# Performance work log

Hardware: AMD Instinct MI355X
Metric: run time of the kernel (lower is better)

## Reference

```python
import jax, jax.numpy as jnp
import numpy as np

BIG = 1e9
GRAPH_LAYERS = 2
FLOW_ITERS = 10
DUAL_ITERS = 10
STEP = 0.1
MOM = 0.9


def _forward(node_features, node_embeddings, demands, adj, neighborhoods,
             enc_W0, enc_b0, enc_W1, enc_b1,
             attn_W, attn_a_src, attn_a_dst, nbr_q,
             gru_W, gru_U, gru_b,
             dec_W0, dec_b0, dec_W1, dec_b1,
             dual_W0, dual_b0, dual_W1, dual_b1):
    E = enc_W1.shape[1]
    K = neighborhoods.shape[0]
    # --- node encoder MLP (tanh, activate_final=True) ---
    x = jnp.concatenate([node_embeddings, node_features], axis=-1)  # [B,N,Fin]
    h = jnp.tanh(jnp.tanh(x @ enc_W0 + enc_b0) @ enc_W1 + enc_b1)   # [B,N,E]
    attn_coefs = None
    for _ in range(GRAPH_LAYERS):
        # --- AttentionNeighborhood: multi-head GAT per hop level, then attention over levels ---
        z = jnp.einsum('bnd,hde->hbne', h, attn_W)                   # [H,B,N,E]
        s_src = jnp.einsum('hbne,he->hbn', z, attn_a_src)
        s_dst = jnp.einsum('hbne,he->hbn', z, attn_a_dst)
        scores = jnp.tanh(s_src[:, :, :, None] + s_dst[:, :, None, :])  # [H,B,N,N]
        aggs = []
        for k in range(K):
            masked = jnp.where(neighborhoods[k][None] > 0, scores, -BIG)
            alpha = jax.nn.softmax(masked, axis=-1)                  # [H,B,N,N]
            agg = jnp.tanh(jnp.einsum('hbnm,hbme->hbne', alpha, z).mean(axis=0))  # heads averaged -> [B,N,E]
            aggs.append(agg)
        aggs = jnp.stack(aggs, axis=2)                               # [B,N,K,E]
        attn_coefs = jax.nn.softmax(jnp.tanh(jnp.einsum('bnke,e->bnk', aggs, nbr_q)), axis=-1)
        nxt = jnp.einsum('bnk,bnke->bne', attn_coefs, aggs)          # [B,N,E]
        # --- GRU state update (tanh activation) ---
        zr = jax.nn.sigmoid(nxt @ gru_W[:, :2 * E] + h @ gru_U[:, :2 * E] + gru_b[:2 * E])
        zg, r = zr[..., :E], zr[..., E:]
        h_tilde = jnp.tanh(nxt @ gru_W[:, 2 * E:] + (r * h) @ gru_U[:, 2 * E:] + gru_b[2 * E:])
        h = (1.0 - zg) * h + zg * h_tilde
    # --- flow-proportion decoder + masked softmax over neighbors ---
    node_weights = jnp.tanh(h @ dec_W0 + dec_b0) @ dec_W1 + dec_b1   # [B,N,1]
    pred = adj * jnp.swapaxes(node_weights, 1, 2)                    # adj * node_weights^T
    weights = -BIG * (1.0 - adj) + pred
    prop = jax.nn.softmax(weights, axis=-1)                          # [B,N,N]
    # --- iterative min-cost-flow solver ---
    def mcf_step(flow, _):
        inflow = flow.sum(axis=1)[:, :, None]                        # inflow_i = sum_j flow[j,i]
        return prop * jax.nn.relu(inflow - demands), None
    flow, _ = jax.lax.scan(mcf_step, jnp.zeros_like(prop), None, length=FLOW_ITERS)
    # should_correct_flows: cancel opposing flow on each edge pair
    flow = flow - adj * jnp.minimum(flow, jnp.swapaxes(flow, 1, 2))
    flow_cost = jnp.sum(flow * flow, axis=(1, 2))                    # square cost, per graph
    # --- dual decoder + projected momentum ascent dual-flow solver ---
    dual_vars = jnp.tanh(h @ dual_W0 + dual_b0) @ dual_W1 + dual_b1  # [B,N,1]
    dual_diff = adj * (dual_vars - jnp.swapaxes(dual_vars, 1, 2))    # [B,N,N]
    def dual_step(carry, _):
        y, m = carry
        g = 2.0 * y - dual_diff                                      # d/dy [y^2 - dual_diff*y]
        m = MOM * m + g
        y = adj * jax.nn.relu(y - STEP * m)
        return (y, m), None
    (dflow, _m), _ = jax.lax.scan(dual_step,
                                  (jnp.zeros_like(dual_diff), jnp.zeros_like(dual_diff)),
                                  None, length=DUAL_ITERS)
    dual_demand = jnp.sum(dual_vars * demands, axis=(1, 2))
    dual_cost = jnp.sum(dflow * dflow - dual_diff * dflow, axis=(1, 2)) - dual_demand
    return flow_cost - dual_cost                                     # primal-dual gap loss, [B]


def setup_inputs() -> dict:
    key = jax.random.key(0)
    ks = jax.random.split(key, 24)
    B, N, Femb, Ffeat, E, H = 2, 2048, 16, 2, 64, 2
    Fin = Femb + Ffeat
    node_embeddings = jax.random.normal(ks[0], (B, N, Femb), jnp.float32)
    node_features = jax.random.normal(ks[1], (B, N, Ffeat), jnp.float32)
    d = jax.random.normal(ks[2], (B, N, 1), jnp.float32) * 0.1
    demands = d - d.mean(axis=1, keepdims=True)                      # balanced demands
    eye = jnp.eye(N, dtype=jnp.float32)
    u = jax.random.uniform(ks[3], (B, N, N))
    adj = (u < 0.008).astype(jnp.float32) * (1.0 - eye)              # avg degree ~16
    a2 = (jnp.matmul(adj, adj) > 0).astype(jnp.float32) * (1.0 - eye)
    neighborhoods = jnp.stack([adj, a2], axis=0)                     # [K,B,N,N]
    def init(k, fan_in, shape):
        return jax.random.normal(k, shape, jnp.float32) / jnp.sqrt(float(fan_in))
    return {
        'node_features': node_features, 'node_embeddings': node_embeddings,
        'demands': demands, 'adj': adj, 'neighborhoods': neighborhoods,
        'enc_W0': init(ks[4], Fin, (Fin, 64)), 'enc_b0': jnp.zeros((64,)),
        'enc_W1': init(ks[5], 64, (64, E)), 'enc_b1': jnp.zeros((E,)),
        'attn_W': init(ks[6], E, (H, E, E)),
        'attn_a_src': init(ks[7], E, (H, E)), 'attn_a_dst': init(ks[8], E, (H, E)),
        'nbr_q': init(ks[9], E, (E,)),
        'gru_W': init(ks[10], E, (E, 3 * E)), 'gru_U': init(ks[11], E, (E, 3 * E)),
        'gru_b': jnp.zeros((3 * E,)),
        'dec_W0': init(ks[12], E, (E, 64)), 'dec_b0': jnp.zeros((64,)),
        'dec_W1': init(ks[13], 64, (64, 1)), 'dec_b1': jnp.zeros((1,)),
        'dual_W0': init(ks[14], E, (E, 64)), 'dual_b0': jnp.zeros((64,)),
        'dual_W1': init(ks[15], 64, (64, 1)), 'dual_b1': jnp.zeros((1,)),
    }


def reference(node_features, node_embeddings, demands, adj, neighborhoods,
              enc_W0, enc_b0, enc_W1, enc_b1,
              attn_W, attn_a_src, attn_a_dst, nbr_q,
              gru_W, gru_U, gru_b,
              dec_W0, dec_b0, dec_W1, dec_b1,
              dual_W0, dual_b0, dual_W1, dual_b1):
    return _forward(node_features, node_embeddings, demands, adj, neighborhoods,
                    enc_W0, enc_b0, enc_W1, enc_b1,
                    attn_W, attn_a_src, attn_a_dst, nbr_q,
                    gru_W, gru_U, gru_b,
                    dec_W0, dec_b0, dec_W1, dec_b1,
                    dual_W0, dual_b0, dual_W1, dual_b1)
```

## Files before the change

kernel.cpp:

```cpp
#include <hip/hip_runtime.h>

#define B_ 2
#define N_ 2048
#define E_ 64
#define FIN_ 18
#define ADJ_CAP 128
#define A2_CAP 1024
#define DR 16

__device__ __forceinline__ float wave_sum(float v) {
  #pragma unroll
  for (int o = 32; o > 0; o >>= 1) v += __shfl_xor(v, o);
  return v;
}
__device__ __forceinline__ float wave_max(float v) {
  #pragma unroll
  for (int o = 32; o > 0; o >>= 1) v = fmaxf(v, __shfl_xor(v, o));
  return v;
}
__device__ __forceinline__ void grp_reduce(float4& a) {
  #pragma unroll
  for (int o = 16; o <= 32; o <<= 1) {
    a.x += __shfl_xor(a.x, o); a.y += __shfl_xor(a.y, o);
    a.z += __shfl_xor(a.z, o); a.w += __shfl_xor(a.w, o);
  }
}

__global__ void k_csr_adj(const float* __restrict__ nbhd, int* __restrict__ adj_idx,
                          int* __restrict__ adj_cnt, unsigned* __restrict__ amask,
                          float* __restrict__ accum, int* __restrict__ tcnt) {
  int wv = threadIdx.x >> 6;
  int row = blockIdx.x * 4 + wv;
  int lane = threadIdx.x & 63;
  if (row == 0 && lane < 8) accum[lane] = 0.f;
  if (lane == 0) tcnt[row] = 0;
  __shared__ unsigned M[4][64];
  M[wv][lane] = 0;
  const float* r = nbhd + (size_t)row * N_;
  int* idx = adj_idx + (size_t)row * ADJ_CAP;
  int cnt = 0;
  unsigned long long below = (1ull << lane) - 1ull;
  for (int j0 = 0; j0 < N_; j0 += 256) {
    float4 v = ((const float4*)(r + j0))[lane];
    bool p0 = v.x > 0.f, p1 = v.y > 0.f, p2 = v.z > 0.f, p3 = v.w > 0.f;
    unsigned long long b0 = __ballot(p0), b1 = __ballot(p1),
                       b2 = __ballot(p2), b3 = __ballot(p3);
    int pos = cnt + __popcll(b0 & below) + __popcll(b1 & below) +
              __popcll(b2 & below) + __popcll(b3 & below);
    int base_j = j0 + lane * 4;
    if (p0) { if (pos < ADJ_CAP) idx[pos] = base_j;     pos++; }
    if (p1) { if (pos < ADJ_CAP) idx[pos] = base_j + 1; pos++; }
    if (p2) { if (pos < ADJ_CAP) idx[pos] = base_j + 2; pos++; }
    if (p3) { if (pos < ADJ_CAP) idx[pos] = base_j + 3; pos++; }
    unsigned nib = (p0 ? 1u : 0u) | (p1 ? 2u : 0u) | (p2 ? 4u : 0u) | (p3 ? 8u : 0u);
    if (nib) atomicOr(&M[wv][(j0 >> 5) + (lane >> 3)], nib << ((lane & 7) * 4));
    cnt += __popcll(b0) + __popcll(b1) + __popcll(b2) + __popcll(b3);
  }
  if (lane == 0) adj_cnt[row] = (cnt < ADJ_CAP) ? cnt : ADJ_CAP;
  amask[(size_t)row * 64 + lane] = M[wv][lane];
}

__global__ __launch_bounds__(64) void k_a2(
    const int* __restrict__ adj_idx, const int* __restrict__ adj_cnt,
    const unsigned* __restrict__ amask, int* __restrict__ a2_idx,
    int* __restrict__ a2_cnt) {
  int row = blockIdx.x;
  int lane = threadIdx.x;
  int base = (row >> 11) * N_;
  int cnt = adj_cnt[row];
  const int* idx = adj_idx + (size_t)row * ADJ_CAP;
  unsigned m = 0;
  for (int t = 0; t < cnt; t++) {
    int j = idx[t];
    m |= amask[(size_t)(base + j) * 64 + lane];
  }
  int i = row & (N_ - 1);
  if ((i >> 5) == lane) m &= ~(1u << (i & 31));
  int pc = __popc(m);
  int pre = pc;
  #pragma unroll
  for (int o = 1; o < 64; o <<= 1) {
    int t2 = __shfl_up(pre, o);
    if (lane >= o) pre += t2;
  }
  int total = __shfl(pre, 63);
  int k = pre - pc;
  int* out = a2_idx + (size_t)row * A2_CAP;
  int colbase = lane * 32;
  while (m) {
    int bit = __ffs(m) - 1;
    if (k < A2_CAP) out[k] = colbase + bit;
    k++;
    m &= m - 1;
  }
  if (lane == 63) a2_cnt[row] = (total < A2_CAP) ? total : A2_CAP;
}

__global__ __launch_bounds__(256) void k_enc(
    const float* __restrict__ emb, const float* __restrict__ feat,
    const float* __restrict__ W0, const float* __restrict__ b0,
    const float* __restrict__ W1, const float* __restrict__ b1,
    float* __restrict__ h) {
  int tid = threadIdx.x, w = tid >> 6, j = tid & 63;
  int row0 = blockIdx.x * DR;
  __shared__ float XL[DR][FIN_];
  __shared__ float HID[DR][64];
  for (int t = tid; t < DR * FIN_; t += 256) {
    int r = t / FIN_, d = t - r * FIN_;
    int row = row0 + r;
    XL[r][d] = (d < 16) ? emb[(size_t)row * 16 + d] : feat[(size_t)row * 2 + (d - 16)];
  }
  __syncthreads();
  float acc[4];
  float b0j = b0[j];
  #pragma unroll
  for (int r = 0; r < 4; r++) acc[r] = b0j;
  #pragma unroll 2
  for (int d = 0; d < FIN_; d++) {
    float wv = W0[d * 64 + j];
    #pragma unroll
    for (int r = 0; r < 4; r++) acc[r] += XL[w * 4 + r][d] * wv;
  }
  #pragma unroll
  for (int r = 0; r < 4; r++) HID[w * 4 + r][j] = tanhf(acc[r]);
  float b1j = b1[j];
  #pragma unroll
  for (int r = 0; r < 4; r++) acc[r] = b1j;
  for (int dq = 0; dq < 16; dq++) {
    float w0 = W1[(4 * dq + 0) * 64 + j];
    float w1 = W1[(4 * dq + 1) * 64 + j];
    float w2 = W1[(4 * dq + 2) * 64 + j];
    float w3 = W1[(4 * dq + 3) * 64 + j];
    #pragma unroll
    for (int r = 0; r < 4; r++) {
      float4 x = ((const float4*)HID[w * 4 + r])[dq];
      acc[r] += x.x * w0 + x.y * w1 + x.z * w2 + x.w * w3;
    }
  }
  #pragma unroll
  for (int r = 0; r < 4; r++)
    h[(size_t)(row0 + w * 4 + r) * 64 + j] = tanhf(acc[r]);
}

__global__ __launch_bounds__(256) void k_z(
    const float* __restrict__ h, const float* __restrict__ attn_W,
    const float* __restrict__ a_src, const float* __restrict__ a_dst,
    float* __restrict__ z, float* __restrict__ ssrc2, float* __restrict__ sdst2) {
  int tid = threadIdx.x, w = tid >> 6, j = tid & 63;
  int head = w & 1, rbase = (w >> 1) * 8;
  int row0 = blockIdx.x * DR;
  __shared__ float HL[DR][64];
  for (int t = tid; t < DR * 64; t += 256) HL[t >> 6][t & 63] = h[(size_t)row0 * 64 + t];
  __syncthreads();
  const float* W = attn_W + head * 64 * 64;
  float acc[8];
  #pragma unroll
  for (int r = 0; r < 8; r++) acc[r] = 0.f;
  for (int dq = 0; dq < 16; dq++) {
    float w0 = W[(4 * dq + 0) * 64 + j];
    float w1 = W[(4 * dq + 1) * 64 + j];
    float w2 = W[(4 * dq + 2) * 64 + j];
    float w3 = W[(4 * dq + 3) * 64 + j];
    #pragma unroll
    for (int r = 0; r < 8; r++) {
      float4 x = ((const float4*)HL[rbase + r])[dq];
      acc[r] += x.x * w0 + x.y * w1 + x.z * w2 + x.w * w3;
    }
  }
  float as = a_src[head * 64 + j], ad = a_dst[head * 64 + j];
  #pragma unroll
  for (int r = 0; r < 8; r++) {
    int row = row0 + rbase + r;
    z[((size_t)head * (B_ * N_) + row) * 64 + j] = acc[r];
    float rs = wave_sum(acc[r] * as), rd = wave_sum(acc[r] * ad);
    if (j == 0) {
      ssrc2[(size_t)row * 2 + head] = rs;
      sdst2[(size_t)row * 2 + head] = rd;
    }
  }
}

__global__ __launch_bounds__(512) void k_agg(
    const int* __restrict__ adj_idx, const int* __restrict__ adj_cnt,
    const int* __restrict__ a2_idx, const int* __restrict__ a2_cnt,
    const float* __restrict__ z, const float* __restrict__ ssrc2,
    const float* __restrict__ sdst2, float* __restrict__ aggs) {
  int tid = threadIdx.x, w = tid >> 6, lane = tid & 63;
  if (blockIdx.x >= B_ * N_) {
    if (w != 0) return;
    int row = blockIdx.x - B_ * N_;
    int b = row >> 11;
    int cnt = adj_cnt[row];
    const int* idx = adj_idx + (size_t)row * ADJ_CAP;
    float2 ss = ((const float2*)ssrc2)[row];
    const float2* sd = (const float2*)sdst2 + (size_t)b * N_;
    int col0 = 0, col1 = 0;
    float e00 = 0.f, e10 = 0.f, e01 = 0.f, e11 = 0.f;
    if (lane < cnt) {
      col0 = idx[lane]; float2 s = sd[col0];
      e00 = __expf(tanhf(ss.x + s.x)); e10 = __expf(tanhf(ss.y + s.y));
    }
    if (lane + 64 < cnt) {
      col1 = idx[lane + 64]; float2 s = sd[col1];
      e01 = __expf(tanhf(ss.x + s.x)); e11 = __expf(tanhf(ss.y + s.y));
    }
    float tot0 = wave_sum(e00 + e01), tot1 = wave_sum(e10 + e11);
    float inv0 = (tot0 > 0.f) ? 1.f / tot0 : 0.f;
    float inv1 = (tot1 > 0.f) ? 1.f / tot1 : 0.f;
    const float* z0 = z + (size_t)b * N_ * 64;
    const float* z1 = z + ((size_t)(B_ * N_) + b * N_) * 64;
    int g = lane >> 4, li = lane & 15;
    float4 a0 = {0.f, 0.f, 0.f, 0.f}, a1 = {0.f, 0.f, 0.f, 0.f};
    for (int j0 = 0; j0 < 64; j0 += 4) {
      if (j0 >= cnt) break;
      int j = j0 + g;
      int c = __shfl(col0, j);
      float e0 = __shfl(e00, j), e1 = __shfl(e10, j);
      if (j < cnt) {
        float4 v0 = ((const float4*)(z0 + (size_t)c * 64))[li];
        float4 v1 = ((const float4*)(z1 + (size_t)c * 64))[li];
        a0.x += e0 * v0.x; a0.y += e0 * v0.y; a0.z += e0 * v0.z; a0.w += e0 * v0.w;
        a1.x += e1 * v1.x; a1.y += e1 * v1.y; a1.z += e1 * v1.z; a1.w += e1 * v1.w;
      }
    }
    if (cnt > 64) {
      for (int j0 = 0; j0 < 64; j0 += 4) {
        if (64 + j0 >= cnt) break;
        int j = j0 + g;
        int c = __shfl(col1, j);
        float e0 = __shfl(e01, j), e1 = __shfl(e11, j);
        if (64 + j < cnt) {
          float4 v0 = ((const float4*)(z0 + (size_t)c * 64))[li];
          float4 v1 = ((const float4*)(z1 + (size_t)c * 64))[li];
          a0.x += e0 * v0.x; a0.y += e0 * v0.y; a0.z += e0 * v0.z; a0.w += e0 * v0.w;
          a1.x += e1 * v1.x; a1.y += e1 * v1.y; a1.z += e1 * v1.z; a1.w += e1 * v1.w;
        }
      }
    }
    grp_reduce(a0); grp_reduce(a1);
    if (g == 0) {
      float4 o;
      o.x = tanhf(0.5f * (a0.x * inv0 + a1.x * inv1));
      o.y = tanhf(0.5f * (a0.y * inv0 + a1.y * inv1));
      o.z = tanhf(0.5f * (a0.z * inv0 + a1.z * inv1));
      o.w = tanhf(0.5f * (a0.w * inv0 + a1.w * inv1));
      ((float4*)(aggs + ((size_t)row * 2 + 0) * 64))[li] = o;
    }
    return;
  }
  int row = blockIdx.x;
  int b = row >> 11;
  int cnt = a2_cnt[row];
  const int* idx = a2_idx + (size_t)row * A2_CAP;
  float2 ss = ((const float2*)ssrc2)[row];
  const float2* sd = (const float2*)sdst2 + (size_t)b * N_;
  int tA = w * 32 + (lane & 31) + (lane >> 5) * 256;
  int tB = tA + 512;
  int colA = 0, colB = 0;
  float eA0 = 0.f, eA1 = 0.f, eB0 = 0.f, eB1 = 0.f;
  float s0 = 0.f, s1 = 0.f;
  if (tA < cnt) {
    colA = idx[tA]; float2 s = sd[colA];
    eA0 = __expf(tanhf(ss.x + s.x)); eA1 = __expf(tanhf(ss.y + s.y));
    s0 += eA0; s1 += eA1;
  }
  if (tB < cnt) {
    colB = idx[tB]; float2 s = sd[colB];
    eB0 = __expf(tanhf(ss.x + s.x)); eB1 = __expf(tanhf(ss.y + s.y));
    s0 += eB0; s1 += eB1;
  }
  s0 = wave_sum(s0); s1 = wave_sum(s1);
  __shared__ float RED[2][8];
  __shared__ float WS0[8][64], WS1[8][64];
  if (lane == 0) { RED[0][w] = s0; RED[1][w] = s1; }
  const float* z0 = z + (size_t)b * N_ * 64;
  const float* z1 = z + ((size_t)(B_ * N_) + b * N_) * 64;
  int g = lane >> 4, li = lane & 15;
  float4 a0 = {0.f, 0.f, 0.f, 0.f}, a1 = {0.f, 0.f, 0.f, 0.f};
  #pragma unroll
  for (int pass = 0; pass < 4; pass++) {
    int half = pass & 1;
    int tbase = (pass >> 1) * 512 + half * 256 + w * 32;
    if (tbase >= cnt) continue;
    for (int j0 = 0; j0 < 32; j0 += 4) {
      if (tbase + j0 >= cnt) break;
      int j = j0 + g;
      int srcl = half * 32 + j;
      int col; float e0, e1;
      if (pass < 2) {
        col = __shfl(colA, srcl); e0 = __shfl(eA0, srcl); e1 = __shfl(eA1, srcl);
      } else {
        col = __shfl(colB, srcl); e0 = __shfl(eB0, srcl); e1 = __shfl(eB1, srcl);
      }
      if (tbase + j < cnt) {
        float4 v0 = ((const float4*)(z0 + (size_t)col * 64))[li];
        float4 v1 = ((const float4*)(z1 + (size_t)col * 64))[li];
        a0.x += e0 * v0.x; a0.y += e0 * v0.y; a0.z += e0 * v0.z; a0.w += e0 * v0.w;
        a1.x += e1 * v1.x; a1.y += e1 * v1.y; a1.z += e1 * v1.z; a1.w += e1 * v1.w;
      }
    }
  }
  grp_reduce(a0); grp_reduce(a1);
  if (g == 0) {
    ((float4*)WS0[w])[li] = a0;
    ((float4*)WS1[w])[li] = a1;
  }
  __syncthreads();
  if (tid < 64) {
    float tot0 = 0.f, tot1 = 0.f, r0 = 0.f, r1 = 0.f;
    #pragma unroll
    for (int q = 0; q < 8; q++) {
      tot0 += RED[0][q]; tot1 += RED[1][q];
      r0 += WS0[q][tid]; r1 += WS1[q][tid];
    }
    float inv0 = (tot0 > 0.f) ? 1.f / tot0 : 0.f;
    float inv1 = (tot1 > 0.f) ? 1.f / tot1 : 0.f;
    aggs[((size_t)row * 2 + 1) * 64 + tid] = tanhf(0.5f * (r0 * inv0 + r1 * inv1));
  }
}

__global__ __launch_bounds__(256) void k_comb(
    const float* __restrict__ aggs, const float* __restrict__ nbr_q,
    const float* __restrict__ gru_W, const float* __restrict__ gru_U,
    const float* __restrict__ gru_b, float* __restrict__ h) {
  int tid = threadIdx.x, w = tid >> 6, j = tid & 63;
  int row0 = blockIdx.x * DR;
  __shared__ float HL[DR][64], NL[DR][64], RGL[DR][64];
  for (int t = tid; t < DR * 64; t += 256) HL[t >> 6][t & 63] = h[(size_t)row0 * 64 + t];
  float q = nbr_q[j];
  #pragma unroll
  for (int r = 0; r < 4; r++) {
    int rr = w * 4 + r, row = row0 + rr;
    float a0 = aggs[((size_t)row * 2 + 0) * 64 + j];
    float a1 = aggs[((size_t)row * 2 + 1) * 64 + j];
    float t0 = tanhf(wave_sum(a0 * q));
    float t1 = tanhf(wave_sum(a1 * q));
    float mx = fmaxf(t0, t1);
    float e0 = __expf(t0 - mx), e1 = __expf(t1 - mx);
    float inv = 1.f / (e0 + e1);
    NL[rr][j] = (e0 * a0 + e1 * a1) * inv;
  }
  __syncthreads();
  float az[4], ar[4];
  float bz = gru_b[j], br = gru_b[64 + j];
  #pragma unroll
  for (int r = 0; r < 4; r++) { az[r] = bz; ar[r] = br; }
  for (int dq = 0; dq < 16; dq++) {
    int d0 = 4 * dq;
    float wz0 = gru_W[(d0 + 0) * 192 + j],      wz1 = gru_W[(d0 + 1) * 192 + j];
    float wz2 = gru_W[(d0 + 2) * 192 + j],      wz3 = gru_W[(d0 + 3) * 192 + j];
    float wr0 = gru_W[(d0 + 0) * 192 + 64 + j], wr1 = gru_W[(d0 + 1) * 192 + 64 + j];
    float wr2 = gru_W[(d0 + 2) * 192 + 64 + j], wr3 = gru_W[(d0 + 3) * 192 + 64 + j];
    float uz0 = gru_U[(d0 + 0) * 192 + j],      uz1 = gru_U[(d0 + 1) * 192 + j];
    float uz2 = gru_U[(d0 + 2) * 192 + j],      uz3 = gru_U[(d0 + 3) * 192 + j];
    float ur0 = gru_U[(d0 + 0) * 192 + 64 + j], ur1 = gru_U[(d0 + 1) * 192 + 64 + j];
    float ur2 = gru_U[(d0 + 2) * 192 + 64 + j], ur3 = gru_U[(d0 + 3) * 192 + 64 + j];
    #pragma unroll
    for (int r = 0; r < 4; r++) {
      float4 n = ((const float4*)NL[w * 4 + r])[dq];
      float4 x = ((const float4*)HL[w * 4 + r])[dq];
      az[r] += n.x * wz0 + n.y * wz1 + n.z * wz2 + n.w * wz3
             + x.x * uz0 + x.y * uz1 + x.z * uz2 + x.w * uz3;
      ar[r] += n.x * wr0 + n.y * wr1 + n.z * wr2 + n.w * wr3
             + x.x * ur0 + x.y * ur1 + x.z * ur2 + x.w * ur3;
    }
  }
  float zgr[4];
  #pragma unroll
  for (int r = 0; r < 4; r++) {
    zgr[r] = 1.f / (1.f + __expf(-az[r]));
    RGL[w * 4 + r][j] = 1.f / (1.f + __expf(-ar[r]));
  }
  float ah[4];
  float bh = gru_b[128 + j];
  #pragma unroll
  for (int r = 0; r < 4; r++) ah[r] = bh;
  for (int dq = 0; dq < 16; dq++) {
    int d0 = 4 * dq;
    float wh0 = gru_W[(d0 + 0) * 192 + 128 + j], wh1 = gru_W[(d0 + 1) * 192 + 128 + j];
    float wh2 = gru_W[(d0 + 2) * 192 + 128 + j], wh3 = gru_W[(d0 + 3) * 192 + 128 + j];
    float uh0 = gru_U[(d0 + 0) * 192 + 128 + j], uh1 = gru_U[(d0 + 1) * 192 + 128 + j];
    float uh2 = gru_U[(d0 + 2) * 192 + 128 + j], uh3 = gru_U[(d0 + 3) * 192 + 128 + j];
    #pragma unroll
    for (int r = 0; r < 4; r++) {
      float4 n = ((const float4*)NL[w * 4 + r])[dq];
      float4 x = ((const float4*)HL[w * 4 + r])[dq];
      float4 rg = ((const float4*)RGL[w * 4 + r])[dq];
      ah[r] += n.x * wh0 + n.y * wh1 + n.z * wh2 + n.w * wh3
             + rg.x * x.x * uh0 + rg.y * x.y * uh1
             + rg.z * x.z * uh2 + rg.w * x.w * uh3;
    }
  }
  #pragma unroll
  for (int r = 0; r < 4; r++) {
    int rr = w * 4 + r;
    float ht = tanhf(ah[r]);
    float hj = HL[rr][j];
    h[(size_t)(row0 + rr) * 64 + j] = (1.f - zgr[r]) * hj + zgr[r] * ht;
  }
}

__global__ __launch_bounds__(256) void k_dec(
    const float* __restrict__ h, const float* __restrict__ dW0,
    const float* __restrict__ db0, const float* __restrict__ dW1,
    const float* __restrict__ db1, const float* __restrict__ uW0,
    const float* __restrict__ ub0, const float* __restrict__ uW1,
    const float* __restrict__ ub1, const float* __restrict__ demands,
    float* __restrict__ nw, float* __restrict__ dv, float* accum) {
  int tid = threadIdx.x, w = tid >> 6, j = tid & 63;
  int row0 = blockIdx.x * DR;
  __shared__ float HL[DR][64];
  __shared__ float DD[4];
  for (int t = tid; t < DR * 64; t += 256) HL[t >> 6][t & 63] = h[(size_t)row0 * 64 + t];
  __syncthreads();
  float accd[4], accu[4];
  float db0j = db0[j], ub0j = ub0[j];
  #pragma unroll
  for (int r = 0; r < 4; r++) { accd[r] = db0j; accu[r] = ub0j; }
  for (int dq = 0; dq < 16; dq++) {
    int d0 = 4 * dq;
    float dw0 = dW0[(d0 + 0) * 64 + j], dw1 = dW0[(d0 + 1) * 64 + j];
    float dw2 = dW0[(d0 + 2) * 64 + j], dw3 = dW0[(d0 + 3) * 64 + j];
    float uw0 = uW0[(d0 + 0) * 64 + j], uw1 = uW0[(d0 + 1) * 64 + j];
    float uw2 = uW0[(d0 + 2) * 64 + j], uw3 = uW0[(d0 + 3) * 64 + j];
    #pragma unroll
    for (int r = 0; r < 4; r++) {
      float4 x = ((const float4*)HL[w * 4 + r])[dq];
      accd[r] += x.x * dw0 + x.y * dw1 + x.z * dw2 + x.w * dw3;
      accu[r] += x.x * uw0 + x.y * uw1 + x.z * uw2 + x.w * uw3;
    }
  }
  float dw1c = dW1[j], uw1c = uW1[j];
  float db1s = db1[0], ub1s = ub1[0];
  float ddl = 0.f;
  #pragma unroll
  for (int r = 0; r < 4; r++) {
    int row = row0 + w * 4 + r;
    float a = wave_sum(tanhf(accd[r]) * dw1c);
    float bb = wave_sum(tanhf(accu[r]) * uw1c);
    if (j == 0) {
      float dvv = bb + ub1s;
      nw[row] = a + db1s; dv[row] = dvv;
      ddl += dvv * demands[row];
    }
  }
  if (j == 0) DD[w] = ddl;
  __syncthreads();
  if (tid == 0) atomicAdd(&accum[4 + (row0 >> 11)], DD[0] + DD[1] + DD[2] + DD[3]);
}

__global__ void k_propT(const int* __restrict__ adj_idx, const int* __restrict__ adj_cnt,
                        const float* __restrict__ nw, const float* __restrict__ demands,
                        float* __restrict__ Pval, int* __restrict__ tcnt,
                        int* __restrict__ tsrc, float* __restrict__ tval,
                        float* __restrict__ sA) {
  int row = blockIdx.x;
  int lane = threadIdx.x;
  int b = row >> 11;
  int base = b * N_;
  int cnt = adj_cnt[row];
  const int* idx = adj_idx + (size_t)row * ADJ_CAP;
  int c0 = (lane < cnt) ? idx[lane] : -1;
  int c1 = (lane + 64 < cnt) ? idx[lane + 64] : -1;
  float v0 = (c0 >= 0) ? nw[base + c0] : -1e30f;
  float v1 = (c1 >= 0) ? nw[base + c1] : -1e30f;
  float m = wave_max(fmaxf(v0, v1));
  float e0 = (c0 >= 0) ? __expf(v0 - m) : 0.f;
  float e1 = (c1 >= 0) ? __expf(v1 - m) : 0.f;
  float s = wave_sum(e0 + e1);
  float inv = (s > 0.f) ? 1.f / s : 0.f;
  float p0 = e0 * inv, p1 = e1 * inv;
  if (c0 >= 0) {
    Pval[(size_t)row * ADJ_CAP + lane] = p0;
    int col = base + c0;
    int pos = atomicAdd(&tcnt[col], 1);
    if (pos < ADJ_CAP) {
      tsrc[(size_t)col * ADJ_CAP + pos] = row;
      tval[(size_t)col * ADJ_CAP + pos] = p0;
    }
  }
  if (c1 >= 0) {
    Pval[(size_t)row * ADJ_CAP + lane + 64] = p1;
    int col = base + c1;
    int pos = atomicAdd(&tcnt[col], 1);
    if (pos < ADJ_CAP) {
      tsrc[(size_t)col * ADJ_CAP + pos] = row;
      tval[(size_t)col * ADJ_CAP + pos] = p1;
    }
  }
  if (lane == 0) sA[row] = fmaxf(-demands[row], 0.f);
}

__global__ __launch_bounds__(256) void k_mcf_iter(
    const int* __restrict__ tcnt, const int* __restrict__ tsrc,
    const float* __restrict__ tval, const float* __restrict__ demands,
    const float* __restrict__ s_in, float* __restrict__ s_out) {
  int j = blockIdx.x * 256 + threadIdx.x;
  int cnt = tcnt[j];
  const int* src = tsrc + (size_t)j * ADJ_CAP;
  const float* val = tval + (size_t)j * ADJ_CAP;
  float c = 0.f;
  int c4 = cnt >> 2;
  for (int q = 0; q < c4; q++) {
    int4 s4 = ((const int4*)src)[q];
    float4 v4 = ((const float4*)val)[q];
    c += v4.x * s_in[s4.x] + v4.y * s_in[s4.y] + v4.z * s_in[s4.z] + v4.w * s_in[s4.w];
  }
  for (int t = c4 * 4; t < cnt; t++) c += val[t] * s_in[src[t]];
  s_out[j] = fmaxf(c - demands[j], 0.f);
}

__global__ __launch_bounds__(256) void k_flowdual(
    const int* __restrict__ adj_idx, const int* __restrict__ adj_cnt,
    const float* __restrict__ Pval, const float* __restrict__ s,
    const float* __restrict__ dv, float* accum) {
  int tid = threadIdx.x;
  int lane = tid & 63, w = tid >> 6;
  int r16 = lane >> 4, e = lane & 15;
  int row = blockIdx.x * 16 + w * 4 + r16;
  int b = row >> 11, i = row & (N_ - 1);
  int cnt = adj_cnt[row];
  float si = s[row], dvi = dv[row];
  const int* idx = adj_idx + (size_t)row * ADJ_CAP;
  const float* pv = Pval + (size_t)row * ADJ_CAP;
  float fc = 0.f, dc = 0.f;
  for (int t = e; t < cnt; t += 16) {
    int j = idx[t];
    float f_ij = si * pv[t];
    const int* jidx = adj_idx + (size_t)(b * N_ + j) * ADJ_CAP;
    int jcnt = adj_cnt[b * N_ + j];
    int lo = 0, hi = jcnt, pos = -1;
    while (lo < hi) {
      int mid = (lo + hi) >> 1;
      int v = jidx[mid];
      if (v == i) { pos = mid; break; }
      if (v < i) lo = mid + 1; else hi = mid;
    }
    float f_ji = (pos >= 0) ? s[b * N_ + j] * Pval[(size_t)(b * N_ + j) * ADJ_CAP + pos] : 0.f;
    float fin = f_ij - fminf(f_ij, f_ji);
    fc += fin * fin;
    float dd = dvi - dv[b * N_ + j];
    float y = 0.f, m = 0.f;
    #pragma unroll
    for (int q = 0; q < 10; q++) {
      float g = 2.f * y - dd;
      m = 0.9f * m + g;
      y = fmaxf(y - 0.1f * m, 0.f);
    }
    dc += y * y - dd * y;
  }
  fc = wave_sum(fc); dc = wave_sum(dc);
  __shared__ float FB[4], DB[4];
  if (lane == 0) { FB[w] = fc; DB[w] = dc; }
  __syncthreads();
  if (tid == 0) {
    int bb = (blockIdx.x * 16) >> 11;
    atomicAdd(&accum[bb], FB[0] + FB[1] + FB[2] + FB[3]);
    atomicAdd(&accum[2 + bb], DB[0] + DB[1] + DB[2] + DB[3]);
  }
}

__global__ void k_fin(const float* accum, float* out) {
  int b = threadIdx.x;
  if (b < B_) out[b] = accum[b] - accum[2 + b] + accum[4 + b];
}

extern "C" void kernel_launch(void* const* d_in, const int* in_sizes, int n_in,
                              void* d_out, int out_size, void* d_ws, size_t ws_size,
                              hipStream_t stream) {
  const float* feat    = (const float*)d_in[0];
  const float* emb     = (const float*)d_in[1];
  const float* demands = (const float*)d_in[2];
  const float* nbhd    = (const float*)d_in[4];
  const float* enc_W0  = (const float*)d_in[5];
  const float* enc_b0  = (const float*)d_in[6];
  const float* enc_W1  = (const float*)d_in[7];
  const float* enc_b1  = (const float*)d_in[8];
  const float* attn_W  = (const float*)d_in[9];
  const float* a_src   = (const float*)d_in[10];
  const float* a_dst   = (const float*)d_in[11];
  const float* nbr_q   = (const float*)d_in[12];
  const float* gru_W   = (const float*)d_in[13];
  const float* gru_U   = (const float*)d_in[14];
  const float* gru_b   = (const float*)d_in[15];
  const float* dec_W0  = (const float*)d_in[16];
  const float* dec_b0  = (const float*)d_in[17];
  const float* dec_W1  = (const float*)d_in[18];
  const float* dec_b1  = (const float*)d_in[19];
  const float* dual_W0 = (const float*)d_in[20];
  const float* dual_b0 = (const float*)d_in[21];
  const float* dual_W1 = (const float*)d_in[22];
  const float* dual_b1 = (const float*)d_in[23];
  float* out = (float*)d_out;

  char* ws = (char*)d_ws;
  size_t off = 0;
  auto alloc = [&](size_t bytes) { char* p = ws + off; off += (bytes + 255) & ~(size_t)255; return p; };
  int*      adj_idx = (int*)     alloc((size_t)B_ * N_ * ADJ_CAP * 4);
  int*      adj_cnt = (int*)     alloc((size_t)B_ * N_ * 4);
  unsigned* amask   = (unsigned*)alloc((size_t)B_ * N_ * 64 * 4);
  int*      a2_idx  = (int*)     alloc((size_t)B_ * N_ * A2_CAP * 4);
  int*      a2_cnt  = (int*)     alloc((size_t)B_ * N_ * 4);
  float*    h       = (float*)   alloc((size_t)B_ * N_ * 64 * 4);
  float*    z       = (float*)   alloc((size_t)2 * B_ * N_ * 64 * 4);
  float*    ssrc2   = (float*)   alloc((size_t)2 * B_ * N_ * 4);
  float*    sdst2   = (float*)   alloc((size_t)2 * B_ * N_ * 4);
  float*    aggs    = (float*)   alloc((size_t)B_ * N_ * 2 * 64 * 4);
  float*    nw      = (float*)   alloc((size_t)B_ * N_ * 4);
  float*    dv      = (float*)   alloc((size_t)B_ * N_ * 4);
  float*    Pval    = (float*)   alloc((size_t)B_ * N_ * ADJ_CAP * 4);
  int*      tcnt    = (int*)     alloc((size_t)B_ * N_ * 4);
  int*      tsrc    = (int*)     alloc((size_t)B_ * N_ * ADJ_CAP * 4);
  float*    tval    = (float*)   alloc((size_t)B_ * N_ * ADJ_CAP * 4);
  float*    sA      = (float*)   alloc((size_t)B_ * N_ * 4);
  float*    sB      = (float*)   alloc((size_t)B_ * N_ * 4);
  float*    accum   = (float*)   alloc(8 * 4);

  k_csr_adj<<<(B_ * N_) / 4, 256, 0, stream>>>(nbhd, adj_idx, adj_cnt, amask, accum, tcnt);
  k_a2<<<B_ * N_, 64, 0, stream>>>(adj_idx, adj_cnt, amask, a2_idx, a2_cnt);
  k_enc<<<(B_ * N_) / DR, 256, 0, stream>>>(emb, feat, enc_W0, enc_b0, enc_W1, enc_b1, h);
  for (int layer = 0; layer < 2; layer++) {
    k_z<<<(B_ * N_) / DR, 256, 0, stream>>>(h, attn_W, a_src, a_dst, z, ssrc2, sdst2);
    k_agg<<<2 * B_ * N_, 512, 0, stream>>>(adj_idx, adj_cnt, a2_idx, a2_cnt,
                                           z, ssrc2, sdst2, aggs);
    k_comb<<<(B_ * N_) / DR, 256, 0, stream>>>(aggs, nbr_q, gru_W, gru_U, gru_b, h);
  }
  k_dec<<<(B_ * N_) / DR, 256, 0, stream>>>(h, dec_W0, dec_b0, dec_W1, dec_b1,
                                            dual_W0, dual_b0, dual_W1, dual_b1,
                                            demands, nw, dv, accum);
  k_propT<<<B_ * N_, 64, 0, stream>>>(adj_idx, adj_cnt, nw, demands, Pval,
                                      tcnt, tsrc, tval, sA);
  for (int it = 0; it < 9; it++) {
    float* sin  = (it & 1) ? sB : sA;
    float* sout = (it & 1) ? sA : sB;
    k_mcf_iter<<<(B_ * N_) / 256, 256, 0, stream>>>(tcnt, tsrc, tval, demands, sin, sout);
  }
  k_flowdual<<<(B_ * N_) / 16, 256, 0, stream>>>(adj_idx, adj_cnt, Pval, sB, dv, accum);
  k_fin<<<1, 64, 0, stream>>>(accum, out);
}
```

Baseline: 381.9 us.

## Fuse MCF tail into one cooperative kernel and split aggregation kernels

The propT, nine mcf iterations, flowdual and final kernels are merged into a single cooperative kernel of 128 blocks that uses grid-wide syncs in place of separate launches. This removes about a dozen launch gaps. The combined aggregation kernel is also split into a 64-thread adjacency kernel and a 256-thread two-hop kernel, so single-wave blocks no longer reserve 512 threads. The trade-off is that grid.sync costs and the small grid may leave much of the GPU idle during the propagation and flow phases.

```diff
diff --git a/kernel.cpp b/kernel.cpp
--- a/kernel.cpp
+++ b/kernel.cpp
@@ -1,4 +1,7 @@
 #include <hip/hip_runtime.h>
+#include <hip/hip_cooperative_groups.h>
+
+namespace cg = cooperative_groups;
 
 #define B_ 2
 #define N_ 2048
@@ -180,119 +183,115 @@
   }
 }
 
-__global__ __launch_bounds__(512) void k_agg(
+__global__ __launch_bounds__(64) void k_agg_adj(
     const int* __restrict__ adj_idx, const int* __restrict__ adj_cnt,
-    const int* __restrict__ a2_idx, const int* __restrict__ a2_cnt,
     const float* __restrict__ z, const float* __restrict__ ssrc2,
     const float* __restrict__ sdst2, float* __restrict__ aggs) {
-  int tid = threadIdx.x, w = tid >> 6, lane = tid & 63;
-  if (blockIdx.x >= B_ * N_) {
-    if (w != 0) return;
-    int row = blockIdx.x - B_ * N_;
-    int b = row >> 11;
-    int cnt = adj_cnt[row];
-    const int* idx = adj_idx + (size_t)row * ADJ_CAP;
-    float2 ss = ((const float2*)ssrc2)[row];
-    const float2* sd = (const float2*)sdst2 + (size_t)b * N_;
-    int col0 = 0, col1 = 0;
-    float e00 = 0.f, e10 = 0.f, e01 = 0.f, e11 = 0.f;
-    if (lane < cnt) {
-      col0 = idx[lane]; float2 s = sd[col0];
-      e00 = __expf(tanhf(ss.x + s.x)); e10 = __expf(tanhf(ss.y + s.y));
-    }
-    if (lane + 64 < cnt) {
-      col1 = idx[lane + 64]; float2 s = sd[col1];
-      e01 = __expf(tanhf(ss.x + s.x)); e11 = __expf(tanhf(ss.y + s.y));
-    }
-    float tot0 = wave_sum(e00 + e01), tot1 = wave_sum(e10 + e11);
-    float inv0 = (tot0 > 0.f) ? 1.f / tot0 : 0.f;
-    float inv1 = (tot1 > 0.f) ? 1.f / tot1 : 0.f;
-    const float* z0 = z + (size_t)b * N_ * 64;
-    const float* z1 = z + ((size_t)(B_ * N_) + b * N_) * 64;
-    int g = lane >> 4, li = lane & 15;
-    float4 a0 = {0.f, 0.f, 0.f, 0.f}, a1 = {0.f, 0.f, 0.f, 0.f};
+  int row = blockIdx.x;
+  int lane = threadIdx.x;
+  int b = row >> 11;
+  int cnt = adj_cnt[row];
+  const int* idx = adj_idx + (size_t)row * ADJ_CAP;
+  float2 ss = ((const float2*)ssrc2)[row];
+  const float2* sd = (const float2*)sdst2 + (size_t)b * N_;
+  int col0 = 0, col1 = 0;
+  float e00 = 0.f, e10 = 0.f, e01 = 0.f, e11 = 0.f;
+  if (lane < cnt) {
+    col0 = idx[lane]; float2 s = sd[col0];
+    e00 = __expf(tanhf(ss.x + s.x)); e10 = __expf(tanhf(ss.y + s.y));
+  }
+  if (lane + 64 < cnt) {
+    col1 = idx[lane + 64]; float2 s = sd[col1];
+    e01 = __expf(tanhf(ss.x + s.x)); e11 = __expf(tanhf(ss.y + s.y));
+  }
+  float tot0 = wave_sum(e00 + e01), tot1 = wave_sum(e10 + e11);
+  float inv0 = (tot0 > 0.f) ? 1.f / tot0 : 0.f;
+  float inv1 = (tot1 > 0.f) ? 1.f / tot1 : 0.f;
+  const float* z0 = z + (size_t)b * N_ * 64;
+  const float* z1 = z + ((size_t)(B_ * N_) + b * N_) * 64;
+  int g = lane >> 4, li = lane & 15;
+  float4 a0 = {0.f, 0.f, 0.f, 0.f}, a1 = {0.f, 0.f, 0.f, 0.f};
+  for (int j0 = 0; j0 < 64; j0 += 4) {
+    if (j0 >= cnt) break;
+    int j = j0 + g;
+    int c = __shfl(col0, j);
+    float e0 = __shfl(e00, j), e1 = __shfl(e10, j);
+    if (j < cnt) {
+      float4 v0 = ((const float4*)(z0 + (size_t)c * 64))[li];
+      float4 v1 = ((const float4*)(z1 + (size_t)c * 64))[li];
+      a0.x += e0 * v0.x; a0.y += e0 * v0.y; a0.z += e0 * v0.z; a0.w += e0 * v0.w;
+      a1.x += e1 * v1.x; a1.y += e1 * v1.y; a1.z += e1 * v1.z; a1.w += e1 * v1.w;
+    }
+  }
+  if (cnt > 64) {
     for (int j0 = 0; j0 < 64; j0 += 4) {
-      if (j0 >= cnt) break;
+      if (64 + j0 >= cnt) break;
       int j = j0 + g;
-      int c = __shfl(col0, j);
-      float e0 = __shfl(e00, j), e1 = __shfl(e10, j);
-      if (j < cnt) {
+      int c = __shfl(col1, j);
+      float e0 = __shfl(e01, j), e1 = __shfl(e11, j);
+      if (64 + j < cnt) {
         float4 v0 = ((const float4*)(z0 + (size_t)c * 64))[li];
         float4 v1 = ((const float4*)(z1 + (size_t)c * 64))[li];
         a0.x += e0 * v0.x; a0.y += e0 * v0.y; a0.z += e0 * v0.z; a0.w += e0 * v0.w;
         a1.x += e1 * v1.x; a1.y += e1 * v1.y; a1.z += e1 * v1.z; a1.w += e1 * v1.w;
       }
     }
-    if (cnt > 64) {
-      for (int j0 = 0; j0 < 64; j0 += 4) {
-        if (64 + j0 >= cnt) break;
-        int j = j0 + g;
-        int c = __shfl(col1, j);
-        float e0 = __shfl(e01, j), e1 = __shfl(e11, j);
-        if (64 + j < cnt) {
-          float4 v0 = ((const float4*)(z0 + (size_t)c * 64))[li];
-          float4 v1 = ((const float4*)(z1 + (size_t)c * 64))[li];
-          a0.x += e0 * v0.x; a0.y += e0 * v0.y; a0.z += e0 * v0.z; a0.w += e0 * v0.w;
-          a1.x += e1 * v1.x; a1.y += e1 * v1.y; a1.z += e1 * v1.z; a1.w += e1 * v1.w;
-        }
-      }
-    }
-    grp_reduce(a0); grp_reduce(a1);
-    if (g == 0) {
-      float4 o;
-      o.x = tanhf(0.5f * (a0.x * inv0 + a1.x * inv1));
-      o.y = tanhf(0.5f * (a0.y * inv0 + a1.y * inv1));
-      o.z = tanhf(0.5f * (a0.z * inv0 + a1.z * inv1));
-      o.w = tanhf(0.5f * (a0.w * inv0 + a1.w * inv1));
-      ((float4*)(aggs + ((size_t)row * 2 + 0) * 64))[li] = o;
-    }
-    return;
-  }
+  }
+  grp_reduce(a0); grp_reduce(a1);
+  if (g == 0) {
+    float4 o;
+    o.x = tanhf(0.5f * (a0.x * inv0 + a1.x * inv1));
+    o.y = tanhf(0.5f * (a0.y * inv0 + a1.y * inv1));
+    o.z = tanhf(0.5f * (a0.z * inv0 + a1.z * inv1));
+    o.w = tanhf(0.5f * (a0.w * inv0 + a1.w * inv1));
+    ((float4*)(aggs + ((size_t)row * 2 + 0) * 64))[li] = o;
+  }
+}
+
+__global__ __launch_bounds__(256) void k_agg_a2(
+    const int* __restrict__ a2_idx, const int* __restrict__ a2_cnt,
+    const float* __restrict__ z, const float* __restrict__ ssrc2,
+    const float* __restrict__ sdst2, float* __restrict__ aggs) {
   int row = blockIdx.x;
+  int tid = threadIdx.x;
+  int w = tid >> 6, lane = tid & 63;
   int b = row >> 11;
   int cnt = a2_cnt[row];
   const int* idx = a2_idx + (size_t)row * A2_CAP;
   float2 ss = ((const float2*)ssrc2)[row];
   const float2* sd = (const float2*)sdst2 + (size_t)b * N_;
-  int tA = w * 32 + (lane & 31) + (lane >> 5) * 256;
-  int tB = tA + 512;
-  int colA = 0, colB = 0;
-  float eA0 = 0.f, eA1 = 0.f, eB0 = 0.f, eB1 = 0.f;
+  int colr[4]; float e0r[4], e1r[4];
   float s0 = 0.f, s1 = 0.f;
-  if (tA < cnt) {
-    colA = idx[tA]; float2 s = sd[colA];
-    eA0 = __expf(tanhf(ss.x + s.x)); eA1 = __expf(tanhf(ss.y + s.y));
-    s0 += eA0; s1 += eA1;
-  }
-  if (tB < cnt) {
-    colB = idx[tB]; float2 s = sd[colB];
-    eB0 = __expf(tanhf(ss.x + s.x)); eB1 = __expf(tanhf(ss.y + s.y));
-    s0 += eB0; s1 += eB1;
+  #pragma unroll
+  for (int c = 0; c < 4; c++) {
+    int t = c * 256 + tid;
+    colr[c] = 0; e0r[c] = 0.f; e1r[c] = 0.f;
+    if (t < cnt) {
+      int cc = idx[t]; colr[c] = cc;
+      float2 s = sd[cc];
+      e0r[c] = __expf(tanhf(ss.x + s.x));
+      e1r[c] = __expf(tanhf(ss.y + s.y));
+      s0 += e0r[c]; s1 += e1r[c];
+    }
   }
   s0 = wave_sum(s0); s1 = wave_sum(s1);
-  __shared__ float RED[2][8];
-  __shared__ float WS0[8][64], WS1[8][64];
+  __shared__ float RED[2][4];
+  __shared__ float WS0[4][64], WS1[4][64];
   if (lane == 0) { RED[0][w] = s0; RED[1][w] = s1; }
   const float* z0 = z + (size_t)b * N_ * 64;
   const float* z1 = z + ((size_t)(B_ * N_) + b * N_) * 64;
   int g = lane >> 4, li = lane & 15;
   float4 a0 = {0.f, 0.f, 0.f, 0.f}, a1 = {0.f, 0.f, 0.f, 0.f};
   #pragma unroll
-  for (int pass = 0; pass < 4; pass++) {
-    int half = pass & 1;
-    int tbase = (pass >> 1) * 512 + half * 256 + w * 32;
-    if (tbase >= cnt) continue;
-    for (int j0 = 0; j0 < 32; j0 += 4) {
-      if (tbase + j0 >= cnt) break;
+  for (int c = 0; c < 4; c++) {
+    int base = c * 256 + w * 64;
+    if (base >= cnt) break;
+    for (int j0 = 0; j0 < 64; j0 += 4) {
+      if (base + j0 >= cnt) break;
       int j = j0 + g;
-      int srcl = half * 32 + j;
-      int col; float e0, e1;
-      if (pass < 2) {
-        col = __shfl(colA, srcl); e0 = __shfl(eA0, srcl); e1 = __shfl(eA1, srcl);
-      } else {
-        col = __shfl(colB, srcl); e0 = __shfl(eB0, srcl); e1 = __shfl(eB1, srcl);
-      }
-      if (tbase + j < cnt) {
+      int col = __shfl(colr[c], j);
+      float e0 = __shfl(e0r[c], j), e1 = __shfl(e1r[c], j);
+      if (base + j < cnt) {
         float4 v0 = ((const float4*)(z0 + (size_t)col * 64))[li];
         float4 v1 = ((const float4*)(z1 + (size_t)col * 64))[li];
         a0.x += e0 * v0.x; a0.y += e0 * v0.y; a0.z += e0 * v0.z; a0.w += e0 * v0.w;
@@ -307,14 +306,12 @@
   }
   __syncthreads();
   if (tid < 64) {
-    float tot0 = 0.f, tot1 = 0.f, r0 = 0.f, r1 = 0.f;
-    #pragma unroll
-    for (int q = 0; q < 8; q++) {
-      tot0 += RED[0][q]; tot1 += RED[1][q];
-      r0 += WS0[q][tid]; r1 += WS1[q][tid];
-    }
+    float tot0 = RED[0][0] + RED[0][1] + RED[0][2] + RED[0][3];
+    float tot1 = RED[1][0] + RED[1][1] + RED[1][2] + RED[1][3];
     float inv0 = (tot0 > 0.f) ? 1.f / tot0 : 0.f;
     float inv1 = (tot1 > 0.f) ? 1.f / tot1 : 0.f;
+    float r0 = WS0[0][tid] + WS0[1][tid] + WS0[2][tid] + WS0[3][tid];
+    float r1 = WS1[0][tid] + WS1[1][tid] + WS1[2][tid] + WS1[3][tid];
     aggs[((size_t)row * 2 + 1) * 64 + tid] = tanhf(0.5f * (r0 * inv0 + r1 * inv1));
   }
 }
@@ -449,120 +446,143 @@
   if (tid == 0) atomicAdd(&accum[4 + (row0 >> 11)], DD[0] + DD[1] + DD[2] + DD[3]);
 }
 
-__global__ void k_propT(const int* __restrict__ adj_idx, const int* __restrict__ adj_cnt,
-                        const float* __restrict__ nw, const float* __restrict__ demands,
-                        float* __restrict__ Pval, int* __restrict__ tcnt,
-                        int* __restrict__ tsrc, float* __restrict__ tval,
-                        float* __restrict__ sA) {
-  int row = blockIdx.x;
-  int lane = threadIdx.x;
-  int b = row >> 11;
-  int base = b * N_;
-  int cnt = adj_cnt[row];
-  const int* idx = adj_idx + (size_t)row * ADJ_CAP;
-  int c0 = (lane < cnt) ? idx[lane] : -1;
-  int c1 = (lane + 64 < cnt) ? idx[lane + 64] : -1;
-  float v0 = (c0 >= 0) ? nw[base + c0] : -1e30f;
-  float v1 = (c1 >= 0) ? nw[base + c1] : -1e30f;
-  float m = wave_max(fmaxf(v0, v1));
-  float e0 = (c0 >= 0) ? __expf(v0 - m) : 0.f;
-  float e1 = (c1 >= 0) ? __expf(v1 - m) : 0.f;
-  float s = wave_sum(e0 + e1);
-  float inv = (s > 0.f) ? 1.f / s : 0.f;
-  float p0 = e0 * inv, p1 = e1 * inv;
-  if (c0 >= 0) {
-    Pval[(size_t)row * ADJ_CAP + lane] = p0;
-    int col = base + c0;
-    int pos = atomicAdd(&tcnt[col], 1);
-    if (pos < ADJ_CAP) {
-      tsrc[(size_t)col * ADJ_CAP + pos] = row;
-      tval[(size_t)col * ADJ_CAP + pos] = p0;
-    }
-  }
-  if (c1 >= 0) {
-    Pval[(size_t)row * ADJ_CAP + lane + 64] = p1;
-    int col = base + c1;
-    int pos = atomicAdd(&tcnt[col], 1);
-    if (pos < ADJ_CAP) {
-      tsrc[(size_t)col * ADJ_CAP + pos] = row;
-      tval[(size_t)col * ADJ_CAP + pos] = p1;
-    }
-  }
-  if (lane == 0) sA[row] = fmaxf(-demands[row], 0.f);
-}
-
-__global__ __launch_bounds__(256) void k_mcf_iter(
-    const int* __restrict__ tcnt, const int* __restrict__ tsrc,
-    const float* __restrict__ tval, const float* __restrict__ demands,
-    const float* __restrict__ s_in, float* __restrict__ s_out) {
-  int j = blockIdx.x * 256 + threadIdx.x;
-  int cnt = tcnt[j];
-  const int* src = tsrc + (size_t)j * ADJ_CAP;
-  const float* val = tval + (size_t)j * ADJ_CAP;
-  float c = 0.f;
-  int c4 = cnt >> 2;
-  for (int q = 0; q < c4; q++) {
-    int4 s4 = ((const int4*)src)[q];
-    float4 v4 = ((const float4*)val)[q];
-    c += v4.x * s_in[s4.x] + v4.y * s_in[s4.y] + v4.z * s_in[s4.z] + v4.w * s_in[s4.w];
-  }
-  for (int t = c4 * 4; t < cnt; t++) c += val[t] * s_in[src[t]];
-  s_out[j] = fmaxf(c - demands[j], 0.f);
-}
-
-__global__ __launch_bounds__(256) void k_flowdual(
+__global__ __launch_bounds__(256) void k_tail(
     const int* __restrict__ adj_idx, const int* __restrict__ adj_cnt,
-    const float* __restrict__ Pval, const float* __restrict__ s,
-    const float* __restrict__ dv, float* accum) {
+    const float* __restrict__ nw, const float* __restrict__ demands,
+    float* __restrict__ Pval, int* __restrict__ tcnt,
+    int* __restrict__ tsrc, float* __restrict__ tval,
+    float* __restrict__ sA, float* __restrict__ sB,
+    const float* __restrict__ dv, float* accum, float* out) {
+  cg::grid_group grid = cg::this_grid();
   int tid = threadIdx.x;
-  int lane = tid & 63, w = tid >> 6;
-  int r16 = lane >> 4, e = lane & 15;
-  int row = blockIdx.x * 16 + w * 4 + r16;
-  int b = row >> 11, i = row & (N_ - 1);
-  int cnt = adj_cnt[row];
-  float si = s[row], dvi = dv[row];
-  const int* idx = adj_idx + (size_t)row * ADJ_CAP;
-  const float* pv = Pval + (size_t)row * ADJ_CAP;
-  float fc = 0.f, dc = 0.f;
-  for (int t = e; t < cnt; t += 16) {
-    int j = idx[t];
-    float f_ij = si * pv[t];
-    const int* jidx = adj_idx + (size_t)(b * N_ + j) * ADJ_CAP;
-    int jcnt = adj_cnt[b * N_ + j];
-    int lo = 0, hi = jcnt, pos = -1;
-    while (lo < hi) {
-      int mid = (lo + hi) >> 1;
-      int v = jidx[mid];
-      if (v == i) { pos = mid; break; }
-      if (v < i) lo = mid + 1; else hi = mid;
-    }
-    float f_ji = (pos >= 0) ? s[b * N_ + j] * Pval[(size_t)(b * N_ + j) * ADJ_CAP + pos] : 0.f;
-    float fin = f_ij - fminf(f_ij, f_ji);
-    fc += fin * fin;
-    float dd = dvi - dv[b * N_ + j];
-    float y = 0.f, m = 0.f;
+  int wv = tid >> 6, lane = tid & 63;
+  int gwave = blockIdx.x * 4 + wv;
+  int gtid = blockIdx.x * 256 + tid;
+  for (int row = gwave; row < B_ * N_; row += 512) {
+    int b = row >> 11;
+    int base = b * N_;
+    int cnt = adj_cnt[row];
+    const int* idx = adj_idx + (size_t)row * ADJ_CAP;
+    int c0 = (lane < cnt) ? idx[lane] : -1;
+    int c1 = (lane + 64 < cnt) ? idx[lane + 64] : -1;
+    float v0 = (c0 >= 0) ? nw[base + c0] : -1e30f;
+    float v1 = (c1 >= 0) ? nw[base + c1] : -1e30f;
+    float m = wave_max(fmaxf(v0, v1));
+    float e0 = (c0 >= 0) ? __expf(v0 - m) : 0.f;
+    float e1 = (c1 >= 0) ? __expf(v1 - m) : 0.f;
+    float s = wave_sum(e0 + e1);
+    float inv = (s > 0.f) ? 1.f / s : 0.f;
+    float p0 = e0 * inv, p1 = e1 * inv;
+    if (c0 >= 0) {
+      Pval[(size_t)row * ADJ_CAP + lane] = p0;
+      int col = base + c0;
+      int pos = atomicAdd(&tcnt[col], 1);
+      if (pos < ADJ_CAP) {
+        tsrc[(size_t)col * ADJ_CAP + pos] = row;
+        tval[(size_t)col * ADJ_CAP + pos] = p0;
+      }
+    }
+    if (c1 >= 0) {
+      Pval[(size_t)row * ADJ_CAP + lane + 64] = p1;
+      int col = base + c1;
+      int pos = atomicAdd(&tcnt[col], 1);
+      if (pos < ADJ_CAP) {
+        tsrc[(size_t)col * ADJ_CAP + pos] = row;
+        tval[(size_t)col * ADJ_CAP + pos] = p1;
+      }
+    }
+    if (lane == 0) sA[row] = fmaxf(-demands[row], 0.f);
+  }
+  __threadfence();
+  grid.sync();
+  int myc = -1, mycnt = 0;
+  const int* msrc = nullptr; const float* mval = nullptr;
+  float mdem = 0.f;
+  if (gtid < B_ * N_) {
+    myc = gtid;
+    mycnt = tcnt[myc];
+    msrc = tsrc + (size_t)myc * ADJ_CAP;
+    mval = tval + (size_t)myc * ADJ_CAP;
+    mdem = demands[myc];
+  }
+  for (int it = 0; it < 9; it++) {
+    const float* sin = (it & 1) ? sB : sA;
+    float* sout = (it & 1) ? sA : sB;
+    if (myc >= 0) {
+      float c = 0.f;
+      int c4 = mycnt >> 2;
+      for (int q = 0; q < c4; q++) {
+        int4 s4 = ((const int4*)msrc)[q];
+        float4 v4 = ((const float4*)mval)[q];
+        c += v4.x * sin[s4.x] + v4.y * sin[s4.y] + v4.z * sin[s4.z] + v4.w * sin[s4.w];
+      }
+      for (int t = c4 * 4; t < mycnt; t++) c += mval[t] * sin[msrc[t]];
+      sout[myc] = fmaxf(c - mdem, 0.f);
+    }
+    __threadfence();
+    grid.sync();
+  }
+  const float* sfin = sB;
+  int grp = gwave * 4 + (lane >> 4);
+  int e = lane & 15;
+  float fcb[2] = {0.f, 0.f}, dcb[2] = {0.f, 0.f};
+  for (int pass = 0; pass < 2; pass++) {
+    int row = grp + pass * 2048;
+    int b = row >> 11, i = row & (N_ - 1);
+    int cnt = adj_cnt[row];
+    float si = sfin[row], dvi = dv[row];
+    const int* idx = adj_idx + (size_t)row * ADJ_CAP;
+    const float* pv = Pval + (size_t)row * ADJ_CAP;
+    float fc = 0.f, dc = 0.f;
+    for (int t = e; t < cnt; t += 16) {
+      int j = idx[t];
+      float f_ij = si * pv[t];
+      const int* jidx = adj_idx + (size_t)(b * N_ + j) * ADJ_CAP;
+      int jcnt = adj_cnt[b * N_ + j];
+      int lo = 0, hi = jcnt, pos = -1;
+      while (lo < hi) {
+        int mid = (lo + hi) >> 1;
+        int v = jidx[mid];
+        if (v == i) { pos = mid; break; }
+        if (v < i) lo = mid + 1; else hi = mid;
+      }
+      float f_ji = (pos >= 0) ? sfin[b * N_ + j] * Pval[(size_t)(b * N_ + j) * ADJ_CAP + pos] : 0.f;
+      float fin = f_ij - fminf(f_ij, f_ji);
+      fc += fin * fin;
+      float dd = dvi - dv[b * N_ + j];
+      float y = 0.f, m = 0.f;
+      #pragma unroll
+      for (int q = 0; q < 10; q++) {
+        float g2 = 2.f * y - dd;
+        m = 0.9f * m + g2;
+        y = fmaxf(y - 0.1f * m, 0.f);
+      }
+      dc += y * y - dd * y;
+    }
+    fcb[b] += fc; dcb[b] += dc;
+  }
+  #pragma unroll
+  for (int o = 1; o < 16; o <<= 1) {
+    fcb[0] += __shfl_xor(fcb[0], o); fcb[1] += __shfl_xor(fcb[1], o);
+    dcb[0] += __shfl_xor(dcb[0], o); dcb[1] += __shfl_xor(dcb[1], o);
+  }
+  __shared__ float R[4][16];
+  int gidx = wv * 4 + (lane >> 4);
+  if (e == 0) {
+    R[0][gidx] = fcb[0]; R[1][gidx] = fcb[1];
+    R[2][gidx] = dcb[0]; R[3][gidx] = dcb[1];
+  }
+  __syncthreads();
+  if (tid < 4) {
+    float s = 0.f;
     #pragma unroll
-    for (int q = 0; q < 10; q++) {
-      float g = 2.f * y - dd;
-      m = 0.9f * m + g;
-      y = fmaxf(y - 0.1f * m, 0.f);
-    }
-    dc += y * y - dd * y;
-  }
-  fc = wave_sum(fc); dc = wave_sum(dc);
-  __shared__ float FB[4], DB[4];
-  if (lane == 0) { FB[w] = fc; DB[w] = dc; }
-  __syncthreads();
-  if (tid == 0) {
-    int bb = (blockIdx.x * 16) >> 11;
-    atomicAdd(&accum[bb], FB[0] + FB[1] + FB[2] + FB[3]);
-    atomicAdd(&accum[2 + bb], DB[0] + DB[1] + DB[2] + DB[3]);
-  }
-}
-
-__global__ void k_fin(const float* accum, float* out) {
-  int b = threadIdx.x;
-  if (b < B_) out[b] = accum[b] - accum[2 + b] + accum[4 + b];
+    for (int q = 0; q < 16; q++) s += R[tid][q];
+    atomicAdd(&accum[(tid & 1) + ((tid >> 1) << 1)], s);
+  }
+  __threadfence();
+  grid.sync();
+  if (blockIdx.x == 0 && tid < B_)
+    out[tid] = accum[tid] - accum[2 + tid] + accum[4 + tid];
 }
 
 extern "C" void kernel_launch(void* const* d_in, const int* in_sizes, int n_in,
@@ -621,20 +641,19 @@
   k_enc<<<(B_ * N_) / DR, 256, 0, stream>>>(emb, feat, enc_W0, enc_b0, enc_W1, enc_b1, h);
   for (int layer = 0; layer < 2; layer++) {
     k_z<<<(B_ * N_) / DR, 256, 0, stream>>>(h, attn_W, a_src, a_dst, z, ssrc2, sdst2);
-    k_agg<<<2 * B_ * N_, 512, 0, stream>>>(adj_idx, adj_cnt, a2_idx, a2_cnt,
-                                           z, ssrc2, sdst2, aggs);
+    k_agg_adj<<<B_ * N_, 64, 0, stream>>>(adj_idx, adj_cnt, z, ssrc2, sdst2, aggs);
+    k_agg_a2<<<B_ * N_, 256, 0, stream>>>(a2_idx, a2_cnt, z, ssrc2, sdst2, aggs);
     k_comb<<<(B_ * N_) / DR, 256, 0, stream>>>(aggs, nbr_q, gru_W, gru_U, gru_b, h);
   }
   k_dec<<<(B_ * N_) / DR, 256, 0, stream>>>(h, dec_W0, dec_b0, dec_W1, dec_b1,
                                             dual_W0, dual_b0, dual_W1, dual_b1,
                                             demands, nw, dv, accum);
-  k_propT<<<B_ * N_, 64, 0, stream>>>(adj_idx, adj_cnt, nw, demands, Pval,
-                                      tcnt, tsrc, tval, sA);
-  for (int it = 0; it < 9; it++) {
-    float* sin  = (it & 1) ? sB : sA;
-    float* sout = (it & 1) ? sA : sB;
-    k_mcf_iter<<<(B_ * N_) / 256, 256, 0, stream>>>(tcnt, tsrc, tval, demands, sin, sout);
-  }
-  k_flowdual<<<(B_ * N_) / 16, 256, 0, stream>>>(adj_idx, adj_cnt, Pval, sB, dv, accum);
-  k_fin<<<1, 64, 0, stream>>>(accum, out);
-}
+  {
+    void* args[] = {
+      (void*)&adj_idx, (void*)&adj_cnt, (void*)&nw, (void*)&demands,
+      (void*)&Pval, (void*)&tcnt, (void*)&tsrc, (void*)&tval,
+      (void*)&sA, (void*)&sB, (void*)&dv, (void*)&accum, (void*)&out
+    };
+    hipLaunchCooperativeKernel((const void*)k_tail, dim3(128), dim3(256), args, 0, stream);
+  }
+}
```

Result: slower. 700.0 us (+83.3%).
